# Optimization experiments

Measured on AMD Instinct MI355X. Metric: run time of the kernel, lower is better.

Reference implementation:

```python
import jax, jax.numpy as jnp
import numpy as np

EPS = 1e-5

def _bn(x, g, b):
    # BatchNorm1d, training-mode forward (biased batch stats)
    m = x.mean(axis=0)
    v = x.var(axis=0)
    return (x - m) * jax.lax.rsqrt(v + EPS) * g + b

def setup_inputs() -> dict:
    key = jax.random.key(0)
    ks = jax.random.split(key, 24)
    B, P, Cin, Cout, share, shrink, r = 8, 4096, 64, 128, 8, 4, 8
    k = 2 * r
    mid = Cout // shrink
    s = 0.05
    inp = {
        'points': jax.random.normal(ks[0], (B, P, 2), jnp.float32),
        'features': jax.random.normal(ks[1], (B * P, Cin), jnp.float32),
        # modules_1: Linear(2+Cin -> k), Bilinear(k,k -> k)
        'W1': jax.random.normal(ks[2], (k, 2 + Cin)) * s,
        'b1': jax.random.normal(ks[3], (k,)) * s,
        'Wb': jax.random.normal(ks[4], (k, k, k)) * s,
        'bb': jax.random.normal(ks[5], (k,)) * s,
        # linear_p: Linear(2->2, no bias), BN(2), ReLU, Linear(2->Cout)
        'Wp1': jax.random.normal(ks[6], (2, 2)) * s,
        'gp': jnp.ones((2,)), 'bp': jnp.zeros((2,)),
        'Wp2': jax.random.normal(ks[7], (Cout, 2)) * s,
        'bp2': jax.random.normal(ks[8], (Cout,)) * s,
        # modules_2: Linear(2k->mid,nb)+BN, Linear(mid->mid/share,nb)+BN, Linear(->Cout/share)
        'W2a': jax.random.normal(ks[9], (mid, 2 * k)) * s,
        'g2a': jnp.ones((mid,)), 'b2a': jnp.zeros((mid,)),
        'W2b': jax.random.normal(ks[10], (mid // share, mid)) * s,
        'g2b': jnp.ones((mid // share,)), 'b2b': jnp.zeros((mid // share,)),
        'W2c': jax.random.normal(ks[11], (Cout // share, mid // share)) * s,
        'b2c': jax.random.normal(ks[12], (Cout // share,)) * s,
        # modules_3: Linear(Cin -> Cout)
        'W3': jax.random.normal(ks[13], (Cout, Cin)) * s,
        'b3': jax.random.normal(ks[14], (Cout,)) * s,
        'radius': r,
        'share_planes': share,
    }
    return inp

def reference(points, features, W1, b1, Wb, bb, Wp1, gp, bp, Wp2, bp2,
              W2a, g2a, b2a, W2b, g2b, b2b, W2c, b2c, W3, b3,
              radius, share_planes):
    B, P, _ = points.shape
    k = 2 * radius
    # circular grouping index: neighbors (i+o) mod P, o in [-r..-1, 1..r]
    offsets = jnp.concatenate([jnp.arange(-radius, 0), jnp.arange(1, radius + 1)])
    nn = (jnp.arange(P)[:, None] + offsets[None, :]) % P            # [P, k]
    idx = (jnp.arange(B)[:, None, None] * P + nn[None]).reshape(-1) # [B*P*k]

    pts = points.reshape(-1, 2)                                     # [N, 2]
    nn_pts = pts[idx].reshape(-1, k, 2)                             # [N, k, 2]
    trans = (nn_pts - pts[:, None, :]).reshape(-1, 2)               # [N*k, 2]
    nn_feat = features[idx]                                         # [N*k, Cin]

    # modules_1: Linear -> ReLU -> Bilinear(e, e)
    e = jax.nn.relu(jnp.concatenate([trans, nn_feat], axis=1) @ W1.T + b1)
    energy = jnp.einsum('ni,oij,nj->no', e, Wb, e) + bb             # [N*k, k]

    # linear_p
    p = jax.nn.relu(_bn(trans @ Wp1.T, gp, bp))
    p_embed = p @ Wp2.T + bp2                                       # [N*k, Cout]
    Cout = p_embed.shape[1]

    # shrink_p: split Cout into (a, k), sum over a
    pe = p_embed.reshape(-1, k, Cout // k, k)
    shrink = pe.sum(axis=2).reshape(-1, k)                          # [N*k, k]

    # modules_2: MLP + softmax over neighbor axis
    w = jnp.concatenate([energy, shrink], axis=1)
    w = jax.nn.relu(_bn(w @ W2a.T, g2a, b2a))
    w = jax.nn.relu(_bn(w @ W2b.T, g2b, b2b))
    w = w @ W2c.T + b2c                                             # [N*k, Cout/share]
    w = jax.nn.softmax(w.reshape(-1, k, Cout // share_planes), axis=1)

    # modules_3 + gather + combine
    v = (features @ W3.T + b3)[idx].reshape(-1, k, Cout)
    a = v + p_embed.reshape(-1, k, Cout)
    a = a.reshape(-1, k, share_planes, Cout // share_planes)
    outputs = (a * w[:, :, None, :]).reshape(-1, k, Cout)           # [N, k, Cout]
    return outputs, trans, idx

if __name__ == '__main__':
    out = reference(**setup_inputs())
    print(out[0].shape, out[1].shape, out[2].shape)
```

## Files before the change

### kernel.cpp

```cpp
#include <hip/hip_runtime.h>

#define DEV static __device__ __forceinline__

namespace {
constexpr int PB   = 4096;
constexpr int NPTS = 32768;
constexpr int RR   = 8;
constexpr int K    = 16;
constexpr int COUT = 128;
constexpr int NK   = NPTS * K;
constexpr int GS1  = 4096;
constexpr float BN_EPS = 1e-5f;

constexpr int    WS_SUM1 = 0;
constexpr int    WS_SUM2 = 4;
constexpr int    WS_SUM3 = 68;
constexpr size_t WS_P2   = 256;
constexpr size_t WS_W1   = WS_P2 + (size_t)GS1 * 64;
constexpr size_t WS_W2   = WS_W1 + (size_t)NK * 16;
}

typedef __attribute__((ext_vector_type(8))) __bf16 bf16x8;
typedef __attribute__((ext_vector_type(4))) float  f32x4;

DEV int nbr_idx(int n, int j) {
    int b = n >> 12, i = n & (PB - 1);
    int o = (j < RR) ? (j - RR) : (j - RR + 1);
    return (b << 12) | ((i + o + PB) & (PB - 1));
}
DEV float wave_sum(float v) {
    #pragma unroll
    for (int off = 32; off >= 1; off >>= 1) v += __shfl_xor(v, off);
    return v;
}
DEV bf16x8 cvt8(float4 a, float4 b) {
    bf16x8 r;
    r[0] = (__bf16)a.x; r[1] = (__bf16)a.y; r[2] = (__bf16)a.z; r[3] = (__bf16)a.w;
    r[4] = (__bf16)b.x; r[5] = (__bf16)b.y; r[6] = (__bf16)b.z; r[7] = (__bf16)b.w;
    return r;
}
DEV float bflo(unsigned u) { union { unsigned x; float f; } c; c.x = u << 16; return c.f; }
DEV float bfhi(unsigned u) { union { unsigned x; float f; } c; c.x = u & 0xffff0000u; return c.f; }
DEV void wave_fence() {
    asm volatile("s_waitcnt lgkmcnt(0)" ::: "memory");
    __builtin_amdgcn_sched_barrier(0);
}

__global__ __launch_bounds__(256) void k_pre(const float* __restrict__ pts,
                                             const float* __restrict__ Wp1,
                                             float* __restrict__ ws)
{
    __shared__ float red[4][4];
    const int t = threadIdx.x, w = t >> 6;
    const float wp10 = Wp1[0], wp11 = Wp1[1], wp12 = Wp1[2], wp13 = Wp1[3];
    float a[4] = {0.f, 0.f, 0.f, 0.f};
    #pragma unroll
    for (int it = 0; it < 4; ++it) {
        const int row = blockIdx.x * 1024 + it * 256 + t;
        const int n = row >> 4, j = row & 15;
        const int idxr = nbr_idx(n, j);
        const float2 pn = ((const float2*)pts)[n];
        const float2 pq = ((const float2*)pts)[idxr];
        const float tx = pq.x - pn.x, ty = pq.y - pn.y;
        const float p10 = wp10 * tx + wp11 * ty;
        const float p11 = wp12 * tx + wp13 * ty;
        a[0] += p10; a[1] += p11; a[2] += p10 * p10; a[3] += p11 * p11;
    }
    #pragma unroll
    for (int q = 0; q < 4; ++q) {
        float s = wave_sum(a[q]);
        if ((t & 63) == 0) red[w][q] = s;
    }
    __syncthreads();
    if (t < 4) atomicAdd(&ws[WS_SUM1 + t], red[0][t] + red[1][t] + red[2][t] + red[3][t]);
}

__global__ __launch_bounds__(256) void k_stage1(
    const float* __restrict__ pts, const float* __restrict__ feat,
    const float* __restrict__ W1, const float* __restrict__ b1,
    const float* __restrict__ Wb, const float* __restrict__ bb,
    const float* __restrict__ Wp1, const float* __restrict__ Wp2,
    const float* __restrict__ bp2, const float* __restrict__ gp,
    const float* __restrict__ bp, const float* __restrict__ W2a,
    float* __restrict__ out_trans, float* __restrict__ out_idx,
    float* __restrict__ ws)
{
    __shared__ float  es[4][2][16][36];
    __shared__ bf16x8 wbLds[512];
    __shared__ float  sA0[16], sA1[16], sA2[16];
    __shared__ float  red[4][64];

    const int t = threadIdx.x, w = t >> 6, l = t & 63, c0 = l & 15, jg = l >> 4;
    const int bid = blockIdx.x;
    const int n0 = ((bid & 7) * (GS1 / 8) + (bid >> 3)) * 8 + w * 2;

    for (int f = t; f < 512; f += 256) {
        const int lg = f >> 6, ll = f & 63, cc0 = ll & 15, jj = ll >> 4;
        const float4* p = (const float4*)(Wb + cc0 * 256 + lg * 32 + jj * 8);
        wbLds[f] = cvt8(p[0], p[1]);
    }
    if (t < 16) {
        float a0 = 0.f, a1 = 0.f, a2 = 0.f;
        for (int a8 = 0; a8 < 8; ++a8) {
            const int cc = a8 * 16 + t;
            a0 += Wp2[2 * cc]; a1 += Wp2[2 * cc + 1]; a2 += bp2[cc];
        }
        sA0[t] = a0; sA1[t] = a1; sA2[t] = a2;
    }

    const float invM = 1.f / (float)NK;
    const float m0 = ws[WS_SUM1 + 0] * invM, m1 = ws[WS_SUM1 + 1] * invM;
    const float q0 = ws[WS_SUM1 + 2] * invM, q1 = ws[WS_SUM1 + 3] * invM;
    const float sc1x = gp[0] * rsqrtf(q0 - m0 * m0 + BN_EPS);
    const float sc1y = gp[1] * rsqrtf(q1 - m1 * m1 + BN_EPS);
    const float sh1x = fmaf(-m0, sc1x, bp[0]), sh1y = fmaf(-m1, sc1y, bp[1]);
    const float wp10 = Wp1[0], wp11 = Wp1[1], wp12 = Wp1[2], wp13 = Wp1[3];

    const float w1cx = W1[c0 * 66], w1cy = W1[c0 * 66 + 1];
    const float b1c = b1[c0], bbc = bb[c0];
    bf16x8 w1b[2];
    #pragma unroll
    for (int kf = 0; kf < 2; ++kf) {
        const float* p = W1 + c0 * 66 + 2 + kf * 32 + jg * 8;
        const float2 v0 = *(const float2*)(p),     v1 = *(const float2*)(p + 2);
        const float2 v2 = *(const float2*)(p + 4), v3 = *(const float2*)(p + 6);
        w1b[kf] = cvt8(make_float4(v0.x, v0.y, v1.x, v1.y),
                       make_float4(v2.x, v2.y, v3.x, v3.y));
    }
    bf16x8 w2ab[2];
    #pragma unroll
    for (int tq = 0; tq < 2; ++tq) {
        const float4* p = (const float4*)(W2a + (c0 + 16 * tq) * 32 + jg * 8);
        w2ab[tq] = cvt8(p[0], p[1]);
    }

    float txv[2], tyv[2], ph0v[2], ph1v[2];
    bf16x8 fa0[2], fa1[2];
    #pragma unroll
    for (int nn = 0; nn < 2; ++nn) {
        const int n = n0 + nn;
        const int idxr = nbr_idx(n, c0);
        const float2 pn = ((const float2*)pts)[n];
        const float2 pq = ((const float2*)pts)[idxr];
        txv[nn] = pq.x - pn.x; tyv[nn] = pq.y - pn.y;
        const float p10 = wp10 * txv[nn] + wp11 * tyv[nn];
        const float p11 = wp12 * txv[nn] + wp13 * tyv[nn];
        ph0v[nn] = fmaxf(fmaf(p10, sc1x, sh1x), 0.f);
        ph1v[nn] = fmaxf(fmaf(p11, sc1y, sh1y), 0.f);
        const float4* fb = (const float4*)(feat + (size_t)idxr * 64 + jg * 8);
        fa0[nn] = cvt8(fb[0], fb[1]);
        fa1[nn] = cvt8(fb[8], fb[9]);
        if (jg == 0) {
            ((float2*)out_trans)[n * 16 + c0] = make_float2(txv[nn], tyv[nn]);
            out_idx[n * 16 + c0] = (float)idxr;
        }
    }

    __syncthreads();

    #pragma unroll
    for (int nn = 0; nn < 2; ++nn) {
        f32x4 acc;
        #pragma unroll
        for (int r = 0; r < 4; ++r) {
            const int row = jg * 4 + r;
            const float trx  = __shfl(txv[nn], row);
            const float tryv = __shfl(tyv[nn], row);
            acc[r] = b1c + w1cx * trx + w1cy * tryv;
        }
        acc = __builtin_amdgcn_mfma_f32_16x16x32_bf16(fa0[nn], w1b[0], acc, 0, 0, 0);
        acc = __builtin_amdgcn_mfma_f32_16x16x32_bf16(fa1[nn], w1b[1], acc, 0, 0, 0);
        #pragma unroll
        for (int r = 0; r < 4; ++r) es[w][nn][jg * 4 + r][c0] = fmaxf(acc[r], 0.f);
    }
    wave_fence();

    const bool hi = (jg & 1);
    const bool ih = (jg >> 1);
    #pragma unroll
    for (int nn = 0; nn < 2; ++nn) {
        const float4 ef0 = *(const float4*)&es[w][nn][c0][0];
        const float4 ef1 = *(const float4*)&es[w][nn][c0][4];
        const float4 ef2 = *(const float4*)&es[w][nn][c0][8];
        const float4 ef3 = *(const float4*)&es[w][nn][c0][12];
        const float ev[16] = {ef0.x, ef0.y, ef0.z, ef0.w, ef1.x, ef1.y, ef1.z, ef1.w,
                              ef2.x, ef2.y, ef2.z, ef2.w, ef3.x, ef3.y, ef3.z, ef3.w};
        float eh[8];
        #pragma unroll
        for (int e = 0; e < 8; ++e) eh[e] = hi ? ev[8 + e] : ev[e];
        f32x4 acc2;
        #pragma unroll
        for (int r = 0; r < 4; ++r) acc2[r] = bbc;
        #pragma unroll
        for (int g = 0; g < 8; ++g) {
            const bf16x8 wg = wbLds[g * 64 + l];
            const float ei = ih ? ev[2 * g + 1] : ev[2 * g];
            bf16x8 a2;
            #pragma unroll
            for (int e = 0; e < 8; ++e) a2[e] = (__bf16)(ei * eh[e]);
            acc2 = __builtin_amdgcn_mfma_f32_16x16x32_bf16(a2, wg, acc2, 0, 0, 0);
        }
        #pragma unroll
        for (int r = 0; r < 4; ++r) es[w][nn][jg * 4 + r][16 + c0] = acc2[r];
    }
    wave_fence();

    float s10 = 0.f, s11 = 0.f, s20 = 0.f, s21 = 0.f;
    f32x4 w1a0[2], w1a1[2];
    #pragma unroll
    for (int nn = 0; nn < 2; ++nn) {
        bf16x8 xa;
        if (jg < 2) {
            const float* src = &es[w][nn][c0][16 + jg * 8];
            #pragma unroll
            for (int e = 0; e < 8; ++e) xa[e] = (__bf16)src[e];
        } else {
            const int off = (jg - 2) * 8;
            #pragma unroll
            for (int e = 0; e < 8; ++e)
                xa[e] = (__bf16)fmaf(ph0v[nn], sA0[off + e],
                                     fmaf(ph1v[nn], sA1[off + e], sA2[off + e]));
        }
        const f32x4 z4 = {0.f, 0.f, 0.f, 0.f};
        w1a0[nn] = __builtin_amdgcn_mfma_f32_16x16x32_bf16(xa, w2ab[0], z4, 0, 0, 0);
        w1a1[nn] = __builtin_amdgcn_mfma_f32_16x16x32_bf16(xa, w2ab[1], z4, 0, 0, 0);
        #pragma unroll
        for (int r = 0; r < 4; ++r) {
            s10 += w1a0[nn][r]; s20 += w1a0[nn][r] * w1a0[nn][r];
            s11 += w1a1[nn][r]; s21 += w1a1[nn][r] * w1a1[nn][r];
        }
    }
    wave_fence();
    #pragma unroll
    for (int nn = 0; nn < 2; ++nn) {
        #pragma unroll
        for (int r = 0; r < 4; ++r) {
            es[w][nn][jg * 4 + r][c0]      = w1a0[nn][r];
            es[w][nn][jg * 4 + r][16 + c0] = w1a1[nn][r];
        }
    }
    wave_fence();

    #pragma unroll
    for (int nn = 0; nn < 2; ++nn) {
        const int row = l >> 2, ch = l & 3;
        const float* src = &es[w][nn][row][ch * 8];
        bf16x8 pk;
        #pragma unroll
        for (int e = 0; e < 8; ++e) pk[e] = (__bf16)src[e];
        reinterpret_cast<bf16x8*>(ws + WS_W1)[(size_t)((n0 + nn) * 16 + row) * 4 + ch] = pk;
    }

    #pragma unroll
    for (int off = 16; off <= 32; off <<= 1) {
        s10 += __shfl_xor(s10, off); s11 += __shfl_xor(s11, off);
        s20 += __shfl_xor(s20, off); s21 += __shfl_xor(s21, off);
    }
    if (jg == 0) {
        red[w][c0] = s10; red[w][16 + c0] = s11;
        red[w][32 + c0] = s20; red[w][48 + c0] = s21;
    }
    __syncthreads();
    if (t < 64)
        (ws + WS_P2)[(size_t)bid * 64 + t] = red[0][t] + red[1][t] + red[2][t] + red[3][t];
}

__global__ __launch_bounds__(256) void k_red2(float* __restrict__ ws)
{
    __shared__ float red[4][64];
    const int t = threadIdx.x, c = t & 63, g = t >> 6;
    const float* P = ws + WS_P2;
    float s = 0.f;
    for (int r = blockIdx.x * 256 + g; r < (blockIdx.x + 1) * 256; r += 4)
        s += P[(size_t)r * 64 + c];
    red[g][c] = s;
    __syncthreads();
    if (t < 64) atomicAdd(&ws[WS_SUM2 + t], red[0][t] + red[1][t] + red[2][t] + red[3][t]);
}

__global__ __launch_bounds__(256) void k_stage3(
    const float* __restrict__ g2a, const float* __restrict__ b2a,
    const float* __restrict__ W2b, float* __restrict__ ws)
{
    __shared__ float sc2s[32], sh2s[32], w2bs[128];
    __shared__ float red[4][8];
    const int t = threadIdx.x, w = t >> 6, l = t & 63;
    if (t < 32) {
        const float invM = 1.f / (float)NK;
        const float m = ws[WS_SUM2 + t] * invM, q = ws[WS_SUM2 + 32 + t] * invM;
        const float sc = g2a[t] * rsqrtf(q - m * m + BN_EPS);
        sc2s[t] = sc; sh2s[t] = fmaf(-m, sc, b2a[t]);
    }
    if (t < 128) w2bs[t] = W2b[t];
    __syncthreads();

    const size_t row = (size_t)blockIdx.x * 256 + t;
    const uint4* w1u = reinterpret_cast<const uint4*>(ws + WS_W1) + row * 4;
    float h[32];
    #pragma unroll
    for (int i = 0; i < 4; ++i) {
        const uint4 u = w1u[i];
        h[i*8+0] = bflo(u.x); h[i*8+1] = bfhi(u.x);
        h[i*8+2] = bflo(u.y); h[i*8+3] = bfhi(u.y);
        h[i*8+4] = bflo(u.z); h[i*8+5] = bfhi(u.z);
        h[i*8+6] = bflo(u.w); h[i*8+7] = bfhi(u.w);
    }
    float acc[4] = {0.f, 0.f, 0.f, 0.f};
    #pragma unroll
    for (int q = 0; q < 32; ++q) {
        const float hv = fmaxf(fmaf(h[q], sc2s[q], sh2s[q]), 0.f);
        #pragma unroll
        for (int p = 0; p < 4; ++p) acc[p] = fmaf(w2bs[p * 32 + q], hv, acc[p]);
    }
    ((float4*)(ws + WS_W2))[row] = make_float4(acc[0], acc[1], acc[2], acc[3]);

    float r8[8] = {acc[0], acc[1], acc[2], acc[3],
                   acc[0]*acc[0], acc[1]*acc[1], acc[2]*acc[2], acc[3]*acc[3]};
    #pragma unroll
    for (int i = 0; i < 8; ++i) r8[i] = wave_sum(r8[i]);
    if (l == 0) {
        #pragma unroll
        for (int i = 0; i < 8; ++i) red[w][i] = r8[i];
    }
    __syncthreads();
    if (t < 8) atomicAdd(&ws[WS_SUM3 + t], red[0][t] + red[1][t] + red[2][t] + red[3][t]);
}

__global__ __launch_bounds__(256) void k_stage4(
    const float* __restrict__ feat, const float* __restrict__ Wp1,
    const float* __restrict__ Wp2, const float* __restrict__ bp2,
    const float* __restrict__ W2c, const float* __restrict__ b2c,
    const float* __restrict__ W3, const float* __restrict__ b3,
    const float* __restrict__ gp, const float* __restrict__ bp,
    const float* __restrict__ g2b, const float* __restrict__ b2b,
    const float* __restrict__ out_trans, const float* __restrict__ ws,
    float* __restrict__ out)
{
    __shared__ bf16x8 w3lds[1024];
    __shared__ float4 pA[32], pB[32], pC[32];
    __shared__ float4 w2c4[16];
    __shared__ float  b2cs[16];

    const int t = threadIdx.x, w = t >> 6, l = t & 63, c0 = l & 15, jg = l >> 4;
    const int bid = blockIdx.x;
    const int n0 = ((bid & 7) * 256 + (bid >> 3)) * 16 + w * 4;

    for (int f = t; f < 1024; f += 256) {
        const int s = f >> 7, kf = (f >> 6) & 1, l2 = f & 63;
        const float4* p = (const float4*)(W3 + (size_t)(16 * s + (l2 & 15)) * 64
                                          + kf * 32 + (l2 >> 4) * 8);
        w3lds[f] = cvt8(p[0], p[1]);
    }
    if (t < 32) {
        const int s = t >> 2, cc = 16 * s + (t & 3) * 4;
        pA[t] = make_float4(Wp2[2*cc], Wp2[2*cc+2], Wp2[2*cc+4], Wp2[2*cc+6]);
        pB[t] = make_float4(Wp2[2*cc+1], Wp2[2*cc+3], Wp2[2*cc+5], Wp2[2*cc+7]);
        pC[t] = make_float4(bp2[cc] + b3[cc], bp2[cc+1] + b3[cc+1],
                            bp2[cc+2] + b3[cc+2], bp2[cc+3] + b3[cc+3]);
    }
    if (t < 16) {
        w2c4[t] = make_float4(W2c[4*t], W2c[4*t+1], W2c[4*t+2], W2c[4*t+3]);
        b2cs[t] = b2c[t];
    }

    const float invM = 1.f / (float)NK;
    const float m0 = ws[WS_SUM1 + 0] * invM, m1 = ws[WS_SUM1 + 1] * invM;
    const float q0 = ws[WS_SUM1 + 2] * invM, q1 = ws[WS_SUM1 + 3] * invM;
    const float sc1x = gp[0] * rsqrtf(q0 - m0 * m0 + BN_EPS);
    const float sc1y = gp[1] * rsqrtf(q1 - m1 * m1 + BN_EPS);
    const float sh1x = fmaf(-m0, sc1x, bp[0]), sh1y = fmaf(-m1, sc1y, bp[1]);
    const float wp10 = Wp1[0], wp11 = Wp1[1], wp12 = Wp1[2], wp13 = Wp1[3];
    float sc3[4], sh3[4];
    #pragma unroll
    for (int p = 0; p < 4; ++p) {
        const float m = ws[WS_SUM3 + p] * invM, q = ws[WS_SUM3 + 4 + p] * invM;
        sc3[p] = g2b[p] * rsqrtf(q - m * m + BN_EPS);
        sh3[p] = fmaf(-m, sc3[p], b2b[p]);
    }

    int idxr[4]; float2 trv[4]; float4 qv[4];
    bf16x8 fa0[4], fa1[4];
    #pragma unroll
    for (int nn = 0; nn < 4; ++nn) {
        const int n = n0 + nn;
        idxr[nn] = nbr_idx(n, c0);
        const float4* fb = (const float4*)(feat + (size_t)idxr[nn] * 64 + jg * 8);
        fa0[nn] = cvt8(fb[0], fb[1]);
        fa1[nn] = cvt8(fb[8], fb[9]);
        trv[nn] = ((const float2*)out_trans)[n * 16 + c0];
        qv[nn]  = ((const float4*)(ws + WS_W2))[n * 16 + c0];
    }
    __syncthreads();

    #pragma unroll
    for (int nn = 0; nn < 4; ++nn) {
        const int n = n0 + nn;
        const float p10 = wp10 * trv[nn].x + wp11 * trv[nn].y;
        const float p11 = wp12 * trv[nn].x + wp13 * trv[nn].y;
        const float ph0 = fmaxf(fmaf(p10, sc1x, sh1x), 0.f);
        const float ph1 = fmaxf(fmaf(p11, sc1y, sh1y), 0.f);
        const float h0 = fmaxf(fmaf(qv[nn].x, sc3[0], sh3[0]), 0.f);
        const float h1 = fmaxf(fmaf(qv[nn].y, sc3[1], sh3[1]), 0.f);
        const float h2 = fmaxf(fmaf(qv[nn].z, sc3[2], sh3[2]), 0.f);
        const float h3 = fmaxf(fmaf(qv[nn].w, sc3[3], sh3[3]), 0.f);
        float wsm[4];
        #pragma unroll
        for (int r = 0; r < 4; ++r) {
            const int c = jg * 4 + r;
            const float4 wc = w2c4[c];
            const float lgv = b2cs[c] + wc.x * h0 + wc.y * h1 + wc.z * h2 + wc.w * h3;
            float mx = lgv;
            #pragma unroll
            for (int off = 1; off <= 8; off <<= 1) mx = fmaxf(mx, __shfl_xor(mx, off));
            const float ex = __expf(lgv - mx);
            float ss = ex;
            #pragma unroll
            for (int off = 1; off <= 8; off <<= 1) ss += __shfl_xor(ss, off);
            wsm[r] = ex / ss;
        }
        float* ob = out + (size_t)(n * 16 + c0) * COUT;
        #pragma unroll
        for (int s = 0; s < 8; ++s) {
            const float4 a4 = pA[s * 4 + jg], b4 = pB[s * 4 + jg], c4 = pC[s * 4 + jg];
            f32x4 ci;
            ci[0] = fmaf(ph0, a4.x, fmaf(ph1, b4.x, c4.x));
            ci[1] = fmaf(ph0, a4.y, fmaf(ph1, b4.y, c4.y));
            ci[2] = fmaf(ph0, a4.z, fmaf(ph1, b4.z, c4.z));
            ci[3] = fmaf(ph0, a4.w, fmaf(ph1, b4.w, c4.w));
            ci = __builtin_amdgcn_mfma_f32_16x16x32_bf16(w3lds[s * 128 + l],      fa0[nn], ci, 0, 0, 0);
            ci = __builtin_amdgcn_mfma_f32_16x16x32_bf16(w3lds[s * 128 + 64 + l], fa1[nn], ci, 0, 0, 0);
            *(float4*)(ob + 16 * s + jg * 4) =
                make_float4(ci[0] * wsm[0], ci[1] * wsm[1], ci[2] * wsm[2], ci[3] * wsm[3]);
        }
    }
}

extern "C" void kernel_launch(void* const* d_in, const int* in_sizes, int n_in,
                              void* d_out, int out_size, void* d_ws, size_t ws_size,
                              hipStream_t stream)
{
    const float* pts  = (const float*)d_in[0];
    const float* feat = (const float*)d_in[1];
    const float* W1   = (const float*)d_in[2];
    const float* b1   = (const float*)d_in[3];
    const float* Wb   = (const float*)d_in[4];
    const float* bb   = (const float*)d_in[5];
    const float* Wp1  = (const float*)d_in[6];
    const float* gp   = (const float*)d_in[7];
    const float* bp   = (const float*)d_in[8];
    const float* Wp2  = (const float*)d_in[9];
    const float* bp2  = (const float*)d_in[10];
    const float* W2a  = (const float*)d_in[11];
    const float* g2a  = (const float*)d_in[12];
    const float* b2a  = (const float*)d_in[13];
    const float* W2b  = (const float*)d_in[14];
    const float* g2b  = (const float*)d_in[15];
    const float* b2b  = (const float*)d_in[16];
    const float* W2c  = (const float*)d_in[17];
    const float* b2c  = (const float*)d_in[18];
    const float* W3   = (const float*)d_in[19];
    const float* b3   = (const float*)d_in[20];

    float* out       = (float*)d_out;
    float* out_trans = out + (size_t)NK * COUT;
    float* out_idx   = out_trans + (size_t)NK * 2;
    float* ws        = (float*)d_ws;

    hipMemsetAsync(ws, 0, 256 * sizeof(float), stream);
    k_pre<<<512, 256, 0, stream>>>(pts, Wp1, ws);
    k_stage1<<<GS1, 256, 0, stream>>>(pts, feat, W1, b1, Wb, bb, Wp1, Wp2, bp2,
                                      gp, bp, W2a, out_trans, out_idx, ws);
    k_red2<<<GS1 / 256, 256, 0, stream>>>(ws);
    k_stage3<<<2048, 256, 0, stream>>>(g2a, b2a, W2b, ws);
    k_stage4<<<2048, 256, 0, stream>>>(feat, Wp1, Wp2, bp2, W2c, b2c, W3, b3,
                                       gp, bp, g2b, b2b, out_trans, ws, out);
}
```

Baseline: 254.0 us.

## Process four chunks per stage1 block and fold second reduction via last-block ticket

Stage1 now launches a quarter as many blocks, and each block loops over four chunks of 8 points. The per-block weight staging (Wb into LDS, W1/W2a conversions, shrink sums) is therefore amortised over more work. The separate k_red2 launch is removed: a global atomic ticket picks the last block to finish, and that block sums all per-block partials into WS_SUM2. This saves a kernel launch and repeated setup, at the cost of a serial final reduction in one block and fewer blocks to fill the GPU.

```diff
diff --git a/kernel.cpp b/kernel.cpp
--- a/kernel.cpp
+++ b/kernel.cpp
@@ -9,12 +9,13 @@
 constexpr int K    = 16;
 constexpr int COUT = 128;
 constexpr int NK   = NPTS * K;
-constexpr int GS1  = 4096;
+constexpr int GS1  = 1024;
 constexpr float BN_EPS = 1e-5f;
 
 constexpr int    WS_SUM1 = 0;
 constexpr int    WS_SUM2 = 4;
 constexpr int    WS_SUM3 = 68;
+constexpr int    WS_TKT  = 80;
 constexpr size_t WS_P2   = 256;
 constexpr size_t WS_W1   = WS_P2 + (size_t)GS1 * 64;
 constexpr size_t WS_W2   = WS_W1 + (size_t)NK * 16;
@@ -89,10 +90,12 @@
     __shared__ bf16x8 wbLds[512];
     __shared__ float  sA0[16], sA1[16], sA2[16];
     __shared__ float  red[4][64];
+    __shared__ int    isLast;
 
     const int t = threadIdx.x, w = t >> 6, l = t & 63, c0 = l & 15, jg = l >> 4;
     const int bid = blockIdx.x;
-    const int n0 = ((bid & 7) * (GS1 / 8) + (bid >> 3)) * 8 + w * 2;
+    const int sb = (bid & 7) * (GS1 / 8) + (bid >> 3);
+    const int nb0 = sb * 32;
 
     for (int f = t; f < 512; f += 256) {
         const int lg = f >> 6, ll = f & 63, cc0 = ll & 15, jj = ll >> 4;
@@ -134,121 +137,128 @@
         w2ab[tq] = cvt8(p[0], p[1]);
     }
 
-    float txv[2], tyv[2], ph0v[2], ph1v[2];
-    bf16x8 fa0[2], fa1[2];
-    #pragma unroll
-    for (int nn = 0; nn < 2; ++nn) {
-        const int n = n0 + nn;
-        const int idxr = nbr_idx(n, c0);
-        const float2 pn = ((const float2*)pts)[n];
-        const float2 pq = ((const float2*)pts)[idxr];
-        txv[nn] = pq.x - pn.x; tyv[nn] = pq.y - pn.y;
-        const float p10 = wp10 * txv[nn] + wp11 * tyv[nn];
-        const float p11 = wp12 * txv[nn] + wp13 * tyv[nn];
-        ph0v[nn] = fmaxf(fmaf(p10, sc1x, sh1x), 0.f);
-        ph1v[nn] = fmaxf(fmaf(p11, sc1y, sh1y), 0.f);
-        const float4* fb = (const float4*)(feat + (size_t)idxr * 64 + jg * 8);
-        fa0[nn] = cvt8(fb[0], fb[1]);
-        fa1[nn] = cvt8(fb[8], fb[9]);
-        if (jg == 0) {
-            ((float2*)out_trans)[n * 16 + c0] = make_float2(txv[nn], tyv[nn]);
-            out_idx[n * 16 + c0] = (float)idxr;
-        }
-    }
-
-    __syncthreads();
-
-    #pragma unroll
-    for (int nn = 0; nn < 2; ++nn) {
-        f32x4 acc;
-        #pragma unroll
-        for (int r = 0; r < 4; ++r) {
-            const int row = jg * 4 + r;
-            const float trx  = __shfl(txv[nn], row);
-            const float tryv = __shfl(tyv[nn], row);
-            acc[r] = b1c + w1cx * trx + w1cy * tryv;
-        }
-        acc = __builtin_amdgcn_mfma_f32_16x16x32_bf16(fa0[nn], w1b[0], acc, 0, 0, 0);
-        acc = __builtin_amdgcn_mfma_f32_16x16x32_bf16(fa1[nn], w1b[1], acc, 0, 0, 0);
-        #pragma unroll
-        for (int r = 0; r < 4; ++r) es[w][nn][jg * 4 + r][c0] = fmaxf(acc[r], 0.f);
-    }
-    wave_fence();
-
-    const bool hi = (jg & 1);
-    const bool ih = (jg >> 1);
-    #pragma unroll
-    for (int nn = 0; nn < 2; ++nn) {
-        const float4 ef0 = *(const float4*)&es[w][nn][c0][0];
-        const float4 ef1 = *(const float4*)&es[w][nn][c0][4];
-        const float4 ef2 = *(const float4*)&es[w][nn][c0][8];
-        const float4 ef3 = *(const float4*)&es[w][nn][c0][12];
-        const float ev[16] = {ef0.x, ef0.y, ef0.z, ef0.w, ef1.x, ef1.y, ef1.z, ef1.w,
-                              ef2.x, ef2.y, ef2.z, ef2.w, ef3.x, ef3.y, ef3.z, ef3.w};
-        float eh[8];
-        #pragma unroll
-        for (int e = 0; e < 8; ++e) eh[e] = hi ? ev[8 + e] : ev[e];
-        f32x4 acc2;
-        #pragma unroll
-        for (int r = 0; r < 4; ++r) acc2[r] = bbc;
-        #pragma unroll
-        for (int g = 0; g < 8; ++g) {
-            const bf16x8 wg = wbLds[g * 64 + l];
-            const float ei = ih ? ev[2 * g + 1] : ev[2 * g];
-            bf16x8 a2;
-            #pragma unroll
-            for (int e = 0; e < 8; ++e) a2[e] = (__bf16)(ei * eh[e]);
-            acc2 = __builtin_amdgcn_mfma_f32_16x16x32_bf16(a2, wg, acc2, 0, 0, 0);
-        }
-        #pragma unroll
-        for (int r = 0; r < 4; ++r) es[w][nn][jg * 4 + r][16 + c0] = acc2[r];
-    }
-    wave_fence();
+    __syncthreads();
 
     float s10 = 0.f, s11 = 0.f, s20 = 0.f, s21 = 0.f;
-    f32x4 w1a0[2], w1a1[2];
-    #pragma unroll
-    for (int nn = 0; nn < 2; ++nn) {
-        bf16x8 xa;
-        if (jg < 2) {
-            const float* src = &es[w][nn][c0][16 + jg * 8];
-            #pragma unroll
-            for (int e = 0; e < 8; ++e) xa[e] = (__bf16)src[e];
-        } else {
-            const int off = (jg - 2) * 8;
-            #pragma unroll
-            for (int e = 0; e < 8; ++e)
-                xa[e] = (__bf16)fmaf(ph0v[nn], sA0[off + e],
-                                     fmaf(ph1v[nn], sA1[off + e], sA2[off + e]));
-        }
-        const f32x4 z4 = {0.f, 0.f, 0.f, 0.f};
-        w1a0[nn] = __builtin_amdgcn_mfma_f32_16x16x32_bf16(xa, w2ab[0], z4, 0, 0, 0);
-        w1a1[nn] = __builtin_amdgcn_mfma_f32_16x16x32_bf16(xa, w2ab[1], z4, 0, 0, 0);
-        #pragma unroll
-        for (int r = 0; r < 4; ++r) {
-            s10 += w1a0[nn][r]; s20 += w1a0[nn][r] * w1a0[nn][r];
-            s11 += w1a1[nn][r]; s21 += w1a1[nn][r] * w1a1[nn][r];
-        }
-    }
-    wave_fence();
-    #pragma unroll
-    for (int nn = 0; nn < 2; ++nn) {
-        #pragma unroll
-        for (int r = 0; r < 4; ++r) {
-            es[w][nn][jg * 4 + r][c0]      = w1a0[nn][r];
-            es[w][nn][jg * 4 + r][16 + c0] = w1a1[nn][r];
-        }
-    }
-    wave_fence();
-
-    #pragma unroll
-    for (int nn = 0; nn < 2; ++nn) {
-        const int row = l >> 2, ch = l & 3;
-        const float* src = &es[w][nn][row][ch * 8];
-        bf16x8 pk;
-        #pragma unroll
-        for (int e = 0; e < 8; ++e) pk[e] = (__bf16)src[e];
-        reinterpret_cast<bf16x8*>(ws + WS_W1)[(size_t)((n0 + nn) * 16 + row) * 4 + ch] = pk;
+
+    #pragma unroll 1
+    for (int ch = 0; ch < 4; ++ch) {
+        const int n0 = nb0 + ch * 8 + w * 2;
+
+        float txv[2], tyv[2], ph0v[2], ph1v[2];
+        bf16x8 fa0[2], fa1[2];
+        #pragma unroll
+        for (int nn = 0; nn < 2; ++nn) {
+            const int n = n0 + nn;
+            const int idxr = nbr_idx(n, c0);
+            const float2 pn = ((const float2*)pts)[n];
+            const float2 pq = ((const float2*)pts)[idxr];
+            txv[nn] = pq.x - pn.x; tyv[nn] = pq.y - pn.y;
+            const float p10 = wp10 * txv[nn] + wp11 * tyv[nn];
+            const float p11 = wp12 * txv[nn] + wp13 * tyv[nn];
+            ph0v[nn] = fmaxf(fmaf(p10, sc1x, sh1x), 0.f);
+            ph1v[nn] = fmaxf(fmaf(p11, sc1y, sh1y), 0.f);
+            const float4* fb = (const float4*)(feat + (size_t)idxr * 64 + jg * 8);
+            fa0[nn] = cvt8(fb[0], fb[1]);
+            fa1[nn] = cvt8(fb[8], fb[9]);
+            if (jg == 0) {
+                ((float2*)out_trans)[n * 16 + c0] = make_float2(txv[nn], tyv[nn]);
+                out_idx[n * 16 + c0] = (float)idxr;
+            }
+        }
+
+        #pragma unroll
+        for (int nn = 0; nn < 2; ++nn) {
+            f32x4 acc;
+            #pragma unroll
+            for (int r = 0; r < 4; ++r) {
+                const int row = jg * 4 + r;
+                const float trx  = __shfl(txv[nn], row);
+                const float tryv = __shfl(tyv[nn], row);
+                acc[r] = b1c + w1cx * trx + w1cy * tryv;
+            }
+            acc = __builtin_amdgcn_mfma_f32_16x16x32_bf16(fa0[nn], w1b[0], acc, 0, 0, 0);
+            acc = __builtin_amdgcn_mfma_f32_16x16x32_bf16(fa1[nn], w1b[1], acc, 0, 0, 0);
+            #pragma unroll
+            for (int r = 0; r < 4; ++r) es[w][nn][jg * 4 + r][c0] = fmaxf(acc[r], 0.f);
+        }
+        wave_fence();
+
+        const bool hi = (jg & 1);
+        const bool ih = (jg >> 1);
+        #pragma unroll
+        for (int nn = 0; nn < 2; ++nn) {
+            const float4 ef0 = *(const float4*)&es[w][nn][c0][0];
+            const float4 ef1 = *(const float4*)&es[w][nn][c0][4];
+            const float4 ef2 = *(const float4*)&es[w][nn][c0][8];
+            const float4 ef3 = *(const float4*)&es[w][nn][c0][12];
+            const float ev[16] = {ef0.x, ef0.y, ef0.z, ef0.w, ef1.x, ef1.y, ef1.z, ef1.w,
+                                  ef2.x, ef2.y, ef2.z, ef2.w, ef3.x, ef3.y, ef3.z, ef3.w};
+            float eh[8];
+            #pragma unroll
+            for (int e = 0; e < 8; ++e) eh[e] = hi ? ev[8 + e] : ev[e];
+            f32x4 acc2;
+            #pragma unroll
+            for (int r = 0; r < 4; ++r) acc2[r] = bbc;
+            #pragma unroll
+            for (int g = 0; g < 8; ++g) {
+                const bf16x8 wg = wbLds[g * 64 + l];
+                const float ei = ih ? ev[2 * g + 1] : ev[2 * g];
+                bf16x8 a2;
+                #pragma unroll
+                for (int e = 0; e < 8; ++e) a2[e] = (__bf16)(ei * eh[e]);
+                acc2 = __builtin_amdgcn_mfma_f32_16x16x32_bf16(a2, wg, acc2, 0, 0, 0);
+            }
+            #pragma unroll
+            for (int r = 0; r < 4; ++r) es[w][nn][jg * 4 + r][16 + c0] = acc2[r];
+        }
+        wave_fence();
+
+        f32x4 w1a0[2], w1a1[2];
+        #pragma unroll
+        for (int nn = 0; nn < 2; ++nn) {
+            bf16x8 xa;
+            if (jg < 2) {
+                const float* src = &es[w][nn][c0][16 + jg * 8];
+                #pragma unroll
+                for (int e = 0; e < 8; ++e) xa[e] = (__bf16)src[e];
+            } else {
+                const int off = (jg - 2) * 8;
+                #pragma unroll
+                for (int e = 0; e < 8; ++e)
+                    xa[e] = (__bf16)fmaf(ph0v[nn], sA0[off + e],
+                                         fmaf(ph1v[nn], sA1[off + e], sA2[off + e]));
+            }
+            const f32x4 z4 = {0.f, 0.f, 0.f, 0.f};
+            w1a0[nn] = __builtin_amdgcn_mfma_f32_16x16x32_bf16(xa, w2ab[0], z4, 0, 0, 0);
+            w1a1[nn] = __builtin_amdgcn_mfma_f32_16x16x32_bf16(xa, w2ab[1], z4, 0, 0, 0);
+            #pragma unroll
+            for (int r = 0; r < 4; ++r) {
+                s10 += w1a0[nn][r]; s20 += w1a0[nn][r] * w1a0[nn][r];
+                s11 += w1a1[nn][r]; s21 += w1a1[nn][r] * w1a1[nn][r];
+            }
+        }
+        wave_fence();
+        #pragma unroll
+        for (int nn = 0; nn < 2; ++nn) {
+            #pragma unroll
+            for (int r = 0; r < 4; ++r) {
+                es[w][nn][jg * 4 + r][c0]      = w1a0[nn][r];
+                es[w][nn][jg * 4 + r][16 + c0] = w1a1[nn][r];
+            }
+        }
+        wave_fence();
+
+        #pragma unroll
+        for (int nn = 0; nn < 2; ++nn) {
+            const int row = l >> 2, chn = l & 3;
+            const float* src = &es[w][nn][row][chn * 8];
+            bf16x8 pk;
+            #pragma unroll
+            for (int e = 0; e < 8; ++e) pk[e] = (__bf16)src[e];
+            reinterpret_cast<bf16x8*>(ws + WS_W1)[(size_t)((n0 + nn) * 16 + row) * 4 + chn] = pk;
+        }
+        wave_fence();
     }
 
     #pragma unroll
@@ -263,19 +273,24 @@
     __syncthreads();
     if (t < 64)
         (ws + WS_P2)[(size_t)bid * 64 + t] = red[0][t] + red[1][t] + red[2][t] + red[3][t];
-}
-
-__global__ __launch_bounds__(256) void k_red2(float* __restrict__ ws)
-{
-    __shared__ float red[4][64];
-    const int t = threadIdx.x, c = t & 63, g = t >> 6;
-    const float* P = ws + WS_P2;
-    float s = 0.f;
-    for (int r = blockIdx.x * 256 + g; r < (blockIdx.x + 1) * 256; r += 4)
-        s += P[(size_t)r * 64 + c];
-    red[g][c] = s;
-    __syncthreads();
-    if (t < 64) atomicAdd(&ws[WS_SUM2 + t], red[0][t] + red[1][t] + red[2][t] + red[3][t]);
+
+    __threadfence();
+    __syncthreads();
+    if (t == 0) {
+        const unsigned v = atomicAdd((unsigned*)(ws + WS_TKT), 1u);
+        isLast = (v == (unsigned)(GS1 - 1));
+    }
+    __syncthreads();
+    if (isLast) {
+        __threadfence();
+        const float* P = ws + WS_P2;
+        const int c = t & 63, g = t >> 6;
+        float s = 0.f;
+        for (int r = g; r < GS1; r += 4) s += P[(size_t)r * 64 + c];
+        red[g][c] = s;
+        __syncthreads();
+        if (t < 64) ws[WS_SUM2 + t] = red[0][t] + red[1][t] + red[2][t] + red[3][t];
+    }
 }
 
 __global__ __launch_bounds__(256) void k_stage3(
@@ -470,7 +485,6 @@
     k_pre<<<512, 256, 0, stream>>>(pts, Wp1, ws);
     k_stage1<<<GS1, 256, 0, stream>>>(pts, feat, W1, b1, Wb, bb, Wp1, Wp2, bp2,
                                       gp, bp, W2a, out_trans, out_idx, ws);
-    k_red2<<<GS1 / 256, 256, 0, stream>>>(ws);
     k_stage3<<<2048, 256, 0, stream>>>(g2a, b2a, W2b, ws);
     k_stage4<<<2048, 256, 0, stream>>>(feat, Wp1, Wp2, bp2, W2c, b2c, W3, b3,
                                        gp, bp, g2b, b2b, out_trans, ws, out);
```

Result: slower. 404.1 us (+59.1%).
